# Kernel tuning notes

Measured on AMD Instinct MI355X. Metric: run time of the kernel, lower is better.

## Reference

```python
import jax, jax.numpy as jnp
import numpy as np

N = 50000        # nodes
E = 1_600_000    # edges
IN = 64          # in_feats
H = 128          # h_feats
L = 5            # num_layers
G = 512          # graphs in batch
C = 10           # num_classes


def setup_inputs() -> dict:
    key = jax.random.key(0)
    ks = jax.random.split(key, 12)
    s = 0.05
    x = jax.random.normal(ks[0], (N, IN), jnp.float32)
    edge_index = jax.random.randint(ks[1], (2, E), 0, N, dtype=jnp.int32)
    batch = jnp.sort(jax.random.randint(ks[2], (N,), 0, G, dtype=jnp.int32))
    edge_weight = jax.random.uniform(ks[3], (E,), jnp.float32)
    # GatedGraphConv params: per-layer mixing weight + shared GRUCell
    weight = jax.random.normal(ks[4], (L, H, H), jnp.float32) * s
    w_ih = jax.random.normal(ks[5], (3 * H, H), jnp.float32) * s
    w_hh = jax.random.normal(ks[6], (3 * H, H), jnp.float32) * s
    b_ih = jax.random.normal(ks[7], (3 * H,), jnp.float32) * s
    b_hh = jax.random.normal(ks[8], (3 * H,), jnp.float32) * s
    # MLP head
    dense1_w = jax.random.normal(ks[9], (4 * H, H), jnp.float32) * s
    dense1_b = jnp.zeros((4 * H,), jnp.float32)
    dense2_w = jax.random.normal(ks[10], (C, 4 * H), jnp.float32) * s
    dense2_b = jnp.zeros((C,), jnp.float32)
    return dict(x=x, edge_index=edge_index, batch=batch, edge_weight=edge_weight,
                weight=weight, w_ih=w_ih, w_hh=w_hh, b_ih=b_ih, b_hh=b_hh,
                dense1_w=dense1_w, dense1_b=dense1_b,
                dense2_w=dense2_w, dense2_b=dense2_b)


def _gru_cell(m, h, w_ih, w_hh, b_ih, b_hh):
    # torch.nn.GRUCell(input=m, hidden=h)
    gi = m @ w_ih.T + b_ih
    gh = h @ w_hh.T + b_hh
    i_r, i_z, i_n = jnp.split(gi, 3, axis=-1)
    h_r, h_z, h_n = jnp.split(gh, 3, axis=-1)
    r = jax.nn.sigmoid(i_r + h_r)
    z = jax.nn.sigmoid(i_z + h_z)
    n = jnp.tanh(i_n + r * h_n)
    return (1.0 - z) * n + z * h


def reference(x, edge_index, batch, edge_weight, weight, w_ih, w_hh, b_ih, b_hh,
              dense1_w, dense1_b, dense2_w, dense2_b):
    src, dst = edge_index[0], edge_index[1]
    # pad in_feats -> h_feats (PyG GatedGraphConv)
    h = jnp.pad(x, ((0, 0), (0, H - IN)))
    for l in range(L):
        m = h @ weight[l]                          # [N, H]
        msg = m[src] * edge_weight[:, None]        # gather + edge gating [E, H]
        agg = jax.ops.segment_sum(msg, dst, num_segments=N)  # scatter-add
        h = _gru_cell(agg, h, w_ih, w_hh, b_ih, b_hh)
    pooled = jax.ops.segment_max(h, batch, num_segments=G)   # global max pool [G, H]
    # dropout is identity in eval mode
    hid = jax.nn.relu(pooled @ dense1_w.T + dense1_b)
    out = hid @ dense2_w.T + dense2_b
    return out
```

## Files before the change

### kernel.cpp

```cpp
#include <hip/hip_runtime.h>
#include <hip/hip_bf16.h>

#define NN 50000
#define NE 1600000
#define FIN 64
#define H 128
#define NL 5
#define NG 512
#define NC 10

typedef __attribute__((ext_vector_type(8))) short short8;
typedef __attribute__((ext_vector_type(4))) float f32x4;

#define OFF_H2A   0
#define OFF_H2B   3200000
#define OFF_CUR   6400000
#define OFF_OFF   6450176
#define OFF_CSR   6500352
#define OFF_POOL  8500352
#define OFF_FWF   8565888
#define OFF_FWHH  8688768

__device__ __forceinline__ short rne_bf16(float f){
    unsigned u = __float_as_uint(f);
    unsigned r = (u + 0x7FFFu + ((u >> 16) & 1u)) >> 16;
    return (short)r;
}
__device__ __forceinline__ float bf_lo(unsigned v){ return __uint_as_float(v << 16); }
__device__ __forceinline__ float bf_hi(unsigned v){ return __uint_as_float(v & 0xFFFF0000u); }


__global__ void k_hist(const int* __restrict__ ei, int* __restrict__ cnt){
    int e = blockIdx.x*256 + threadIdx.x;
    if (e < NE) atomicAdd(&cnt[ei[NE + e]], 1);
}

__global__ void k_scan(int* __restrict__ cur, int* __restrict__ off){
    __shared__ int s[1024];
    int t = threadIdx.x;
    const int CH = 49;
    int base = t*CH;
    int m = (NN + 1) - base; if (m > CH) m = CH; if (m < 0) m = 0;
    int sum = 0;
    for (int i = 0; i < m; ++i) sum += (cur[base + i] + 7) & ~7;
    s[t] = sum; __syncthreads();
    for (int o = 1; o < 1024; o <<= 1){
        int v = (t >= o) ? s[t - o] : 0; __syncthreads();
        s[t] += v; __syncthreads();
    }
    int run = s[t] - sum;
    for (int i = 0; i < m; ++i){
        int c = (cur[base + i] + 7) & ~7;
        off[base + i] = run;
        cur[base + i] = run;
        run += c;
    }
}

__global__ void k_fill(const int* __restrict__ ei, const float* __restrict__ ew,
                       int* __restrict__ cur, unsigned* __restrict__ csr){
    int e = blockIdx.x*256 + threadIdx.x;
    if (e >= NE) return;
    int src = ei[e], dst = ei[NE + e];
    int pos = atomicAdd(&cur[dst], 1);
    csr[pos] = (unsigned)src | (((unsigned)(ushort)rne_bf16(ew[e])) << 16);
}


__global__ void k_pad(const float* __restrict__ x, ushort* __restrict__ h2a){
    int idx = blockIdx.x*256 + threadIdx.x;
    int n = idx >> 7, f = idx & 127;
    float v = (f < FIN) ? x[n*FIN + f] : 0.f;
    h2a[idx] = (ushort)rne_bf16(v);
}

__global__ void k_fuse(const float* __restrict__ W, const float* __restrict__ wih,
                       short* __restrict__ fwf){
    int idx = blockIdx.x*256 + threadIdx.x;
    int l = idx / 49152;
    int r = idx % 49152;
    int k = r / 384, n = r % 384;
    const float* wl = W + l*16384 + k*128;
    const float* wi = wih + n*128;
    float acc = 0.f;
    for (int c = 0; c < 128; ++c) acc += wl[c]*wi[c];
    int lane = ((k>>3)&3)*16 + (n&15);
    fwf[l*49152 + (((n>>4)*4 + (k>>5))*64 + lane)*8 + (k&7)] = rne_bf16(acc);
}

__global__ void k_cvt_whh(const float* __restrict__ whh, short* __restrict__ fwhh){
    int idx = blockIdx.x*256 + threadIdx.x;
    int k = idx / 384, n = idx % 384;
    float v = whh[n*128 + k];
    int lane = ((k>>3)&3)*16 + (n&15);
    fwhh[(((n>>4)*4 + (k>>5))*64 + lane)*8 + (k&7)] = rne_bf16(v);
}

__global__ void k_init_pool(unsigned* __restrict__ p){
    p[blockIdx.x*256 + threadIdx.x] = 0x007FFFFFu;
}

__global__ __launch_bounds__(256)
void k_layer(const ushort* __restrict__ h2r, ushort* __restrict__ h2w,
             const int* __restrict__ off, const unsigned* __restrict__ csr,
             const short* __restrict__ fwf, const short* __restrict__ fwhh,
             const float* __restrict__ b_ih, const float* __restrict__ b_hh,
             const int* __restrict__ batch, unsigned* __restrict__ pooled,
             int last){
    __shared__ ushort tl[16*136];
    int tid = threadIdx.x;
    int n0 = blockIdx.x * 16;
    int wave = tid >> 6, lane = tid & 63;
    int lane_lo = lane & 15, quad = lane >> 4;

    unsigned* tld = (unsigned*)tl;
    const ushort* hp = h2r + lane*2;
    for (int sub = 0; sub < 4; ++sub){
        int node = n0 + wave*4 + sub;
        int start = __builtin_amdgcn_readfirstlane(off[node]);
        int end   = __builtin_amdgcn_readfirstlane(off[node + 1]);
        float ax = 0.f, ay = 0.f;
        for (int i = start; i < end; i += 8){
            unsigned e0 = csr[i+0], e1 = csr[i+1], e2 = csr[i+2], e3 = csr[i+3];
            unsigned e4 = csr[i+4], e5 = csr[i+5], e6 = csr[i+6], e7 = csr[i+7];
            unsigned v0 = *(const unsigned*)(hp + (e0 & 0xFFFFu)*H);
            unsigned v1 = *(const unsigned*)(hp + (e1 & 0xFFFFu)*H);
            unsigned v2 = *(const unsigned*)(hp + (e2 & 0xFFFFu)*H);
            unsigned v3 = *(const unsigned*)(hp + (e3 & 0xFFFFu)*H);
            unsigned v4 = *(const unsigned*)(hp + (e4 & 0xFFFFu)*H);
            unsigned v5 = *(const unsigned*)(hp + (e5 & 0xFFFFu)*H);
            unsigned v6 = *(const unsigned*)(hp + (e6 & 0xFFFFu)*H);
            unsigned v7 = *(const unsigned*)(hp + (e7 & 0xFFFFu)*H);
            ax += bf_hi(e0)*bf_lo(v0); ay += bf_hi(e0)*bf_hi(v0);
            ax += bf_hi(e1)*bf_lo(v1); ay += bf_hi(e1)*bf_hi(v1);
            ax += bf_hi(e2)*bf_lo(v2); ay += bf_hi(e2)*bf_hi(v2);
            ax += bf_hi(e3)*bf_lo(v3); ay += bf_hi(e3)*bf_hi(v3);
            ax += bf_hi(e4)*bf_lo(v4); ay += bf_hi(e4)*bf_hi(v4);
            ax += bf_hi(e5)*bf_lo(v5); ay += bf_hi(e5)*bf_hi(v5);
            ax += bf_hi(e6)*bf_lo(v6); ay += bf_hi(e6)*bf_hi(v6);
            ax += bf_hi(e7)*bf_lo(v7); ay += bf_hi(e7)*bf_hi(v7);
        }
        tld[(wave*4 + sub)*68 + lane] =
            ((unsigned)(ushort)rne_bf16(ax)) | (((unsigned)(ushort)rne_bf16(ay)) << 16);
    }
    __syncthreads();

    f32x4 ai[6], ah[6];
    #pragma unroll
    for (int i = 0; i < 6; ++i){ ai[i] = (f32x4){0.f,0.f,0.f,0.f}; ah[i] = (f32x4){0.f,0.f,0.f,0.f}; }

    const ushort* arow_t = tl + lane_lo*136;
    const ushort* arow_h = h2r + (size_t)(n0 + lane_lo)*H;
    #pragma unroll
    for (int kt = 0; kt < 4; ++kt){
        short8 at  = *(const short8*)(arow_t + kt*32 + quad*8);
        short8 ahh = *(const short8*)(arow_h + kt*32 + quad*8);
        #pragma unroll
        for (int s = 0; s < 3; ++s){
            #pragma unroll
            for (int t16 = 0; t16 < 2; ++t16){
                int tile = (s*8 + wave*2 + t16)*4 + kt;
                short8 bi = *(const short8*)(fwf  + tile*512 + lane*8);
                short8 bh = *(const short8*)(fwhh + tile*512 + lane*8);
                ai[s*2+t16] = __builtin_amdgcn_mfma_f32_16x16x32_bf16(at,  bi, ai[s*2+t16], 0, 0, 0);
                ah[s*2+t16] = __builtin_amdgcn_mfma_f32_16x16x32_bf16(ahh, bh, ah[s*2+t16], 0, 0, 0);
            }
        }
    }

    #pragma unroll
    for (int t16 = 0; t16 < 2; ++t16){
        int j = wave*32 + t16*16 + lane_lo;
        float bir = b_ih[j], biz = b_ih[128 + j], bin_ = b_ih[256 + j];
        float bhr = b_hh[j], bhz = b_hh[128 + j], bhn  = b_hh[256 + j];
        #pragma unroll
        for (int r = 0; r < 4; ++r){
            int row = n0 + quad*4 + r;
            float gir = ai[t16][r]     + bir, ghr = ah[t16][r]     + bhr;
            float giz = ai[2 + t16][r] + biz, ghz = ah[2 + t16][r] + bhz;
            float gin = ai[4 + t16][r] + bin_, ghn = ah[4 + t16][r] + bhn;
            float rr = 1.f/(1.f + __expf(-(gir + ghr)));
            float zz = 1.f/(1.f + __expf(-(giz + ghz)));
            float nn = tanhf(gin + rr*ghn);
            float ho = __uint_as_float(((unsigned)h2r[(size_t)row*H + j]) << 16);
            float hv = (1.f - zz)*nn + zz*ho;
            if (!last){
                h2w[(size_t)row*H + j] = (ushort)rne_bf16(hv);
            } else {
                int g = batch[row];
                unsigned u = __float_as_uint(hv);
                u = (u & 0x80000000u) ? ~u : (u | 0x80000000u);
                atomicMax(pooled + g*H + j, u);
            }
        }
    }
}


__global__ void k_head(const unsigned* __restrict__ pooled,
                       const float* __restrict__ d1w, const float* __restrict__ d1b,
                       const float* __restrict__ d2w, const float* __restrict__ d2b,
                       float* __restrict__ out){
    __shared__ float sp[128];
    __shared__ float shid[512];
    int g = blockIdx.x, tid = threadIdx.x;
    if (tid < 128){
        unsigned u = pooled[g*H + tid];
        sp[tid] = __uint_as_float((u & 0x80000000u) ? (u ^ 0x80000000u) : ~u);
    }
    __syncthreads();
    for (int o = tid; o < 512; o += 256){
        float acc = d1b[o];
        for (int k = 0; k < H; ++k) acc += sp[k] * d1w[o*H + k];
        shid[o] = fmaxf(acc, 0.f);
    }
    __syncthreads();
    if (tid < NC){
        float acc = d2b[tid];
        for (int o = 0; o < 512; ++o) acc += shid[o] * d2w[tid*512 + o];
        out[g*NC + tid] = acc;
    }
}

extern "C" void kernel_launch(void* const* d_in, const int* in_sizes, int n_in,
                              void* d_out, int out_size, void* d_ws, size_t ws_size,
                              hipStream_t stream){
    const float* x     = (const float*)d_in[0];
    const int*   ei    = (const int*)d_in[1];
    const int*   batch = (const int*)d_in[2];
    const float* ew    = (const float*)d_in[3];
    const float* W     = (const float*)d_in[4];
    const float* wih   = (const float*)d_in[5];
    const float* whh   = (const float*)d_in[6];
    const float* bih   = (const float*)d_in[7];
    const float* bhh   = (const float*)d_in[8];
    const float* d1w   = (const float*)d_in[9];
    const float* d1b   = (const float*)d_in[10];
    const float* d2w   = (const float*)d_in[11];
    const float* d2b   = (const float*)d_in[12];
    float* out = (float*)d_out;

    float*  ws  = (float*)d_ws;
    ushort* h2a = (ushort*)(ws + OFF_H2A);
    ushort* h2b = (ushort*)(ws + OFF_H2B);
    int*    cur = (int*)(ws + OFF_CUR);
    int*    off = (int*)(ws + OFF_OFF);
    unsigned* csr = (unsigned*)(ws + OFF_CSR);
    unsigned* pooled = (unsigned*)(ws + OFF_POOL);
    short*  fwf  = (short*)(ws + OFF_FWF);
    short*  fwhh = (short*)(ws + OFF_FWHH);

    hipMemsetAsync(cur, 0, 50176*sizeof(int), stream);
    hipMemsetAsync(csr, 0, 2000000*sizeof(unsigned), stream);
    k_hist<<<6250, 256, 0, stream>>>(ei, cur);
    k_scan<<<1, 1024, 0, stream>>>(cur, off);
    k_fill<<<6250, 256, 0, stream>>>(ei, ew, cur, csr);

    k_fuse<<<960, 256, 0, stream>>>(W, wih, fwf);
    k_cvt_whh<<<192, 256, 0, stream>>>(whh, fwhh);
    k_pad<<<25000, 256, 0, stream>>>(x, h2a);
    k_init_pool<<<256, 256, 0, stream>>>(pooled);

    for (int l = 0; l < NL; ++l){
        ushort* h2r = (l & 1) ? h2b : h2a;
        ushort* h2w = (l & 1) ? h2a : h2b;
        k_layer<<<3125, 256, 0, stream>>>(h2r, h2w, off, csr,
                                          fwf + (size_t)l*49152, fwhh, bih, bhh,
                                          batch, pooled, (l == NL-1) ? 1 : 0);
    }

    k_head<<<NG, 256, 0, stream>>>(pooled, d1w, d1b, d2w, d2b, out);
}
```

Before: 927.8 us.

## Gather neighbor rows with 16-byte loads split across lane groups

Restructures the edge aggregation so each wave handles 4 edges per step. Each group of 16 lanes loads a 16-byte slice (8 bf16 features) of one neighbor row, and the partial sums are combined with cross-lane shuffles. This replaces the previous scheme where every lane did 4-byte gathers over 8 edges sequentially. CSR padding grows from multiples of 8 to multiples of 16 to match the vector CSR reads, which enlarges the workspace and memset and adds more zero-weight padded edges per node.

```diff
diff --git a/kernel.cpp b/kernel.cpp
--- a/kernel.cpp
+++ b/kernel.cpp
@@ -17,9 +17,9 @@
 #define OFF_CUR   6400000
 #define OFF_OFF   6450176
 #define OFF_CSR   6500352
-#define OFF_POOL  8500352
-#define OFF_FWF   8565888
-#define OFF_FWHH  8688768
+#define OFF_POOL  8900352
+#define OFF_FWF   8965888
+#define OFF_FWHH  9088768
 
 __device__ __forceinline__ short rne_bf16(float f){
     unsigned u = __float_as_uint(f);
@@ -42,7 +42,7 @@
     int base = t*CH;
     int m = (NN + 1) - base; if (m > CH) m = CH; if (m < 0) m = 0;
     int sum = 0;
-    for (int i = 0; i < m; ++i) sum += (cur[base + i] + 7) & ~7;
+    for (int i = 0; i < m; ++i) sum += (cur[base + i] + 15) & ~15;
     s[t] = sum; __syncthreads();
     for (int o = 1; o < 1024; o <<= 1){
         int v = (t >= o) ? s[t - o] : 0; __syncthreads();
@@ -50,7 +50,7 @@
     }
     int run = s[t] - sum;
     for (int i = 0; i < m; ++i){
-        int c = (cur[base + i] + 7) & ~7;
+        int c = (cur[base + i] + 15) & ~15;
         off[base + i] = run;
         cur[base + i] = run;
         run += c;
@@ -112,36 +112,40 @@
     int n0 = blockIdx.x * 16;
     int wave = tid >> 6, lane = tid & 63;
     int lane_lo = lane & 15, quad = lane >> 4;
-
-    unsigned* tld = (unsigned*)tl;
-    const ushort* hp = h2r + lane*2;
+    int grp = lane >> 4, fl = lane & 15;
+
     for (int sub = 0; sub < 4; ++sub){
         int node = n0 + wave*4 + sub;
         int start = __builtin_amdgcn_readfirstlane(off[node]);
         int end   = __builtin_amdgcn_readfirstlane(off[node + 1]);
-        float ax = 0.f, ay = 0.f;
-        for (int i = start; i < end; i += 8){
-            unsigned e0 = csr[i+0], e1 = csr[i+1], e2 = csr[i+2], e3 = csr[i+3];
-            unsigned e4 = csr[i+4], e5 = csr[i+5], e6 = csr[i+6], e7 = csr[i+7];
-            unsigned v0 = *(const unsigned*)(hp + (e0 & 0xFFFFu)*H);
-            unsigned v1 = *(const unsigned*)(hp + (e1 & 0xFFFFu)*H);
-            unsigned v2 = *(const unsigned*)(hp + (e2 & 0xFFFFu)*H);
-            unsigned v3 = *(const unsigned*)(hp + (e3 & 0xFFFFu)*H);
-            unsigned v4 = *(const unsigned*)(hp + (e4 & 0xFFFFu)*H);
-            unsigned v5 = *(const unsigned*)(hp + (e5 & 0xFFFFu)*H);
-            unsigned v6 = *(const unsigned*)(hp + (e6 & 0xFFFFu)*H);
-            unsigned v7 = *(const unsigned*)(hp + (e7 & 0xFFFFu)*H);
-            ax += bf_hi(e0)*bf_lo(v0); ay += bf_hi(e0)*bf_hi(v0);
-            ax += bf_hi(e1)*bf_lo(v1); ay += bf_hi(e1)*bf_hi(v1);
-            ax += bf_hi(e2)*bf_lo(v2); ay += bf_hi(e2)*bf_hi(v2);
-            ax += bf_hi(e3)*bf_lo(v3); ay += bf_hi(e3)*bf_hi(v3);
-            ax += bf_hi(e4)*bf_lo(v4); ay += bf_hi(e4)*bf_hi(v4);
-            ax += bf_hi(e5)*bf_lo(v5); ay += bf_hi(e5)*bf_hi(v5);
-            ax += bf_hi(e6)*bf_lo(v6); ay += bf_hi(e6)*bf_hi(v6);
-            ax += bf_hi(e7)*bf_lo(v7); ay += bf_hi(e7)*bf_hi(v7);
-        }
-        tld[(wave*4 + sub)*68 + lane] =
-            ((unsigned)(ushort)rne_bf16(ax)) | (((unsigned)(ushort)rne_bf16(ay)) << 16);
+        float a0=0.f,a1=0.f,a2=0.f,a3=0.f,a4=0.f,a5=0.f,a6=0.f,a7=0.f;
+        const ushort* hb = h2r + fl*8;
+        for (int i = start; i < end; i += 16){
+            uint4 c = *(const uint4*)(csr + i + grp*4);
+            uint4 v0 = *(const uint4*)(hb + (c.x & 0xFFFFu)*H);
+            uint4 v1 = *(const uint4*)(hb + (c.y & 0xFFFFu)*H);
+            uint4 v2 = *(const uint4*)(hb + (c.z & 0xFFFFu)*H);
+            uint4 v3 = *(const uint4*)(hb + (c.w & 0xFFFFu)*H);
+            float w0 = bf_hi(c.x), w1 = bf_hi(c.y), w2 = bf_hi(c.z), w3 = bf_hi(c.w);
+            a0 += w0*bf_lo(v0.x); a1 += w0*bf_hi(v0.x); a2 += w0*bf_lo(v0.y); a3 += w0*bf_hi(v0.y);
+            a4 += w0*bf_lo(v0.z); a5 += w0*bf_hi(v0.z); a6 += w0*bf_lo(v0.w); a7 += w0*bf_hi(v0.w);
+            a0 += w1*bf_lo(v1.x); a1 += w1*bf_hi(v1.x); a2 += w1*bf_lo(v1.y); a3 += w1*bf_hi(v1.y);
+            a4 += w1*bf_lo(v1.z); a5 += w1*bf_hi(v1.z); a6 += w1*bf_lo(v1.w); a7 += w1*bf_hi(v1.w);
+            a0 += w2*bf_lo(v2.x); a1 += w2*bf_hi(v2.x); a2 += w2*bf_lo(v2.y); a3 += w2*bf_hi(v2.y);
+            a4 += w2*bf_lo(v2.z); a5 += w2*bf_hi(v2.z); a6 += w2*bf_lo(v2.w); a7 += w2*bf_hi(v2.w);
+            a0 += w3*bf_lo(v3.x); a1 += w3*bf_hi(v3.x); a2 += w3*bf_lo(v3.y); a3 += w3*bf_hi(v3.y);
+            a4 += w3*bf_lo(v3.z); a5 += w3*bf_hi(v3.z); a6 += w3*bf_lo(v3.w); a7 += w3*bf_hi(v3.w);
+        }
+        a0 += __shfl_xor(a0,16); a1 += __shfl_xor(a1,16); a2 += __shfl_xor(a2,16); a3 += __shfl_xor(a3,16);
+        a4 += __shfl_xor(a4,16); a5 += __shfl_xor(a5,16); a6 += __shfl_xor(a6,16); a7 += __shfl_xor(a7,16);
+        a0 += __shfl_xor(a0,32); a1 += __shfl_xor(a1,32); a2 += __shfl_xor(a2,32); a3 += __shfl_xor(a3,32);
+        a4 += __shfl_xor(a4,32); a5 += __shfl_xor(a5,32); a6 += __shfl_xor(a6,32); a7 += __shfl_xor(a7,32);
+        if (lane < 16){
+            short8 hbv;
+            hbv[0]=rne_bf16(a0); hbv[1]=rne_bf16(a1); hbv[2]=rne_bf16(a2); hbv[3]=rne_bf16(a3);
+            hbv[4]=rne_bf16(a4); hbv[5]=rne_bf16(a5); hbv[6]=rne_bf16(a6); hbv[7]=rne_bf16(a7);
+            *(short8*)(tl + (wave*4 + sub)*136 + fl*8) = hbv;
+        }
     }
     __syncthreads();
 
@@ -251,7 +255,7 @@
     short*  fwhh = (short*)(ws + OFF_FWHH);
 
     hipMemsetAsync(cur, 0, 50176*sizeof(int), stream);
-    hipMemsetAsync(csr, 0, 2000000*sizeof(unsigned), stream);
+    hipMemsetAsync(csr, 0, 2400000*sizeof(unsigned), stream);
     k_hist<<<6250, 256, 0, stream>>>(ei, cur);
     k_scan<<<1, 1024, 0, stream>>>(cur, off);
     k_fill<<<6250, 256, 0, stream>>>(ei, ew, cur, csr);
```

Result: no change. 920.5 us (-0.8%).
